# Kernel tuning notes

Measured on AMD Instinct MI355X. Metric: run time of the kernel, lower is better.

The kernel has to match this reference:

```python
import jax, jax.numpy as jnp
import numpy as np

B, DIM = 16384, 1024
H1, H2, H3 = 500, 200, 200


def setup_inputs() -> dict:
    key = jax.random.key(0)
    ks = jax.random.split(key, 16)
    s = 0.01
    return {
        "x": jax.random.normal(ks[0], (B, DIM), dtype=jnp.float32),
        "show_index": jax.random.randint(ks[1], (B,), 0, 100),
        "st": jax.random.normal(ks[2], (1000, 16), dtype=jnp.float32),
        # deep MLP params (shared across the two task heads, as in the source)
        "W1": jax.random.normal(ks[3], (DIM, H1), dtype=jnp.float32) * s,
        "b1": jnp.zeros((H1,), dtype=jnp.float32),
        "W2": jax.random.normal(ks[4], (H1, H2), dtype=jnp.float32) * s,
        "b2": jnp.zeros((H2,), dtype=jnp.float32),
        "W3": jax.random.normal(ks[5], (H2, H3), dtype=jnp.float32) * s,
        "b3": jnp.zeros((H3,), dtype=jnp.float32),
        # final sigmoid head on concat([emb(DIM), d3(H3)])
        "Wl": jax.random.normal(ks[6], (DIM + H3, 1), dtype=jnp.float32) * s,
        "bl": jnp.zeros((1,), dtype=jnp.float32),
        # per-(task, cross-layer) cross weights/biases: tf.random_normal stddev=0.01
        "cw": jax.random.normal(ks[7], (2, 3, DIM), dtype=jnp.float32) * s,
        "cb": jax.random.normal(ks[8], (2, 3, DIM), dtype=jnp.float32) * s,
    }


def reference(x, show_index, st, W1, b1, W2, b2, W3, b3, Wl, bl, cw, cb):
    # Deep part (same shared Dense layers each task -> compute once).
    d = jax.nn.relu(x @ W1 + b1)
    d = jax.nn.relu(d @ W2 + b2)
    d3 = jax.nn.relu(d @ W3 + b3)  # (B, H3)

    # cross_net: sum_i w[j] * x[b,i] * emb[b,j]  ==  x.sum(1) * emb[b,j] * w[j]
    # (collapsed form of the (B,dim,dim) outer product + axis-1 reduction)
    xsum = jnp.sum(x, axis=1, keepdims=True)  # (B, 1)
    preds = []
    for i in range(2):
        emb = x
        for j in range(3):
            emb = xsum * emb * cw[i, j] + cb[i, j] + x
        mid = jnp.concatenate([emb, d3], axis=-1)  # (B, DIM+H3)
        preds.append(jax.nn.sigmoid(mid @ Wl + bl))  # (B, 1)
    return tuple(preds)
```

## Files before the change

kernel.cpp:

```cpp
#include <hip/hip_runtime.h>
#include <hip/hip_bf16.h>
#include <math.h>

#define B_ROWS 16384
#define DIM 1024

typedef __attribute__((ext_vector_type(8))) short s16x8;
typedef __attribute__((ext_vector_type(4))) float f32x4;

static __device__ __forceinline__ unsigned short f2bf(float f) {
    union { float f; unsigned u; } v; v.f = f;
    unsigned r = v.u + 0x7FFF + ((v.u >> 16) & 1);
    return (unsigned short)(r >> 16);
}

static __device__ __forceinline__ unsigned f2fp8(float f) {
    union { float f; unsigned u; } v; v.f = f;
    const unsigned s = (v.u >> 24) & 0x80u;
    const float a = fabsf(f);
    if (a >= 448.f) return s | 0x7Eu;
    if (a < 0.015625f) {
        const int q = (int)rintf(a * 512.f);
        return s | (unsigned)q;
    }
    unsigned b = v.u & 0x7fffffffu;
    b += 0x000FFFFFu + ((b >> 20) & 1u);
    const int e = (int)(b >> 23) - 127;
    const unsigned m = (b >> 20) & 7u;
    return s | (unsigned)((e + 7) << 3) | m;
}

static __device__ __forceinline__ unsigned cvt4_fp8(float a, float b, float c, float d) {
    unsigned u;
    asm volatile("v_cvt_pk_fp8_f32 %0, %1, %2\n\t"
                 "v_cvt_pk_fp8_f32 %0, %3, %4 op_sel:[0,0,1]"
                 : "=v"(u) : "v"(a), "v"(b), "v"(c), "v"(d));
    return u;
}

static __device__ __forceinline__ void gload16(const void* g, void* l) {
    __builtin_amdgcn_global_load_lds(
        (const __attribute__((address_space(1))) unsigned int*)g,
        (__attribute__((address_space(3))) unsigned int*)l, 16, 0, 0);
}

__global__ __launch_bounds__(256, 5) void xdots_prep(
    const float* __restrict__ x,
    const float* __restrict__ W1, const float* __restrict__ W2,
    const float* __restrict__ W3,
    const float* __restrict__ cw, const float* __restrict__ cb,
    const float* __restrict__ Wl,
    unsigned char* __restrict__ W1q,
    unsigned short* __restrict__ W2b, unsigned short* __restrict__ W3b,
    float* __restrict__ czz,
    unsigned char* __restrict__ xq,
    float* __restrict__ zparts) {
    __shared__ unsigned short tile[64][72];
    __shared__ unsigned char tilec[64][72];
    __shared__ float red[4][6];
    const int tid  = threadIdx.x;
    const int lane = tid & 63;
    const int w    = tid >> 6;
    const int blk  = blockIdx.x;

    if (blk < 128) {
        const int kt = blk & 15, nt = blk >> 4;
        const int k0 = kt << 6, n0 = nt << 6;
        {
            const int r = tid >> 2, c0 = (tid & 3) << 4;
            const int kk = k0 + r;
#pragma unroll
            for (int i = 0; i < 16; ++i) {
                const int nn = n0 + c0 + i;
                const float v = (nn < 500) ? W1[(size_t)kk * 500 + nn] * 64.f : 0.f;
                tilec[r][c0 + i] = (unsigned char)f2fp8(v);
            }
        }
        __syncthreads();
        {
            const int n = tid >> 2, kc = (tid & 3) << 4;
            unsigned char* o = W1q + (size_t)(n0 + n) * 1024 + k0 + kc;
#pragma unroll
            for (int i = 0; i < 16; ++i) o[i] = tilec[kc + i][n];
        }
        return;
    } else if (blk < 176) {
        const float* src; unsigned short* dst;
        int kt, nt, Ksrc, Nsrc, ldDst;
        if (blk < 160) { kt = (blk - 128) & 7;  nt = (blk - 128) >> 3; src = W2; dst = W2b; Ksrc = 500; Nsrc = 200; ldDst = 512; }
        else           { kt = (blk - 160) & 3;  nt = (blk - 160) >> 2; src = W3; dst = W3b; Ksrc = 200; Nsrc = 200; ldDst = 256; }
        const int k0 = kt << 6, n0 = nt << 6;
        {
            const int r = tid >> 2, c0 = (tid & 3) << 4;
            const int kk = k0 + r;
#pragma unroll
            for (int i = 0; i < 16; ++i) {
                const int nn = n0 + c0 + i;
                const float v = (kk < Ksrc && nn < Nsrc) ? src[(size_t)kk * Nsrc + nn] : 0.f;
                tile[r][c0 + i] = f2bf(v);
            }
        }
        __syncthreads();
        {
            const int n = tid >> 2, kc = (tid & 3) << 4;
            unsigned short* o = dst + (size_t)(n0 + n) * ldDst + k0 + kc;
#pragma unroll
            for (int i = 0; i < 16; ++i) o[i] = tile[kc + i][n];
        }
        return;
    } else if (blk == 176) {
        float c[6] = {0.f, 0.f, 0.f, 0.f, 0.f, 0.f};
#pragma unroll
        for (int q = 0; q < 4; ++q) {
            const int k = tid * 4 + q;
            const float wl = Wl[k];
            {
                const float w2 = cw[1024 + k], w3 = cw[2048 + k];
                const float b1 = cb[k], b2 = cb[1024 + k], b3 = cb[2048 + k];
                c[0] += w2 * w3 * b1 * wl;
                c[1] += w3 * b2 * wl;
                c[2] += b3 * wl;
            }
            {
                const float w2 = cw[4096 + k], w3 = cw[5120 + k];
                const float b1 = cb[3072 + k], b2 = cb[4096 + k], b3 = cb[5120 + k];
                c[3] += w2 * w3 * b1 * wl;
                c[4] += w3 * b2 * wl;
                c[5] += b3 * wl;
            }
        }
#pragma unroll
        for (int j = 0; j < 6; ++j)
#pragma unroll
            for (int m = 1; m < 64; m <<= 1) c[j] += __shfl_xor(c[j], m, 64);
        if (lane == 0)
#pragma unroll
            for (int j = 0; j < 6; ++j) red[w][j] = c[j];
        __syncthreads();
        if (tid < 6) czz[tid] = red[0][tid] + red[1][tid] + red[2][tid] + red[3][tid];
        return;
    }

    const int row0 = (blk - 177) * 8 + (w << 1);
    float d[2][8];
#pragma unroll
    for (int r = 0; r < 2; ++r)
#pragma unroll
        for (int j = 0; j < 8; ++j) d[r][j] = 0.f;

#pragma unroll
    for (int c = 0; c < 4; ++c) {
        const int kb = c * 256 + lane * 4;
        const float4 wl4 = *(const float4*)(Wl + kb);
        const float4 c0 = *(const float4*)(cw + kb);
        const float4 c1 = *(const float4*)(cw + 1024 + kb);
        const float4 c2 = *(const float4*)(cw + 2048 + kb);
        const float4 c3 = *(const float4*)(cw + 3072 + kb);
        const float4 c4 = *(const float4*)(cw + 4096 + kb);
        const float4 c5 = *(const float4*)(cw + 5120 + kb);
        const float4 xv0 = *(const float4*)(x + (size_t)row0 * DIM + kb);
        const float4 xv1 = *(const float4*)(x + (size_t)(row0 + 1) * DIM + kb);

        const float* wlp = (const float*)&wl4;
        const float* p0 = (const float*)&c0; const float* p1 = (const float*)&c1;
        const float* p2 = (const float*)&c2; const float* p3 = (const float*)&c3;
        const float* p4 = (const float*)&c4; const float* p5 = (const float*)&c5;
        const float* xa = (const float*)&xv0; const float* xb = (const float*)&xv1;
#pragma unroll
        for (int q = 0; q < 4; ++q) {
            const float wl  = wlp[q];
            const float pa1 = p2[q] * wl;
            const float pa2 = p1[q] * pa1;
            const float pa3 = p0[q] * pa2;
            const float pb1 = p5[q] * wl;
            const float pb2 = p4[q] * pb1;
            const float pb3 = p3[q] * pb2;
            const float a = xa[q], b = xb[q];
            d[0][0] = fmaf(a, pa3, d[0][0]);
            d[0][1] = fmaf(a, pa2, d[0][1]);
            d[0][2] = fmaf(a, pa1, d[0][2]);
            d[0][3] = fmaf(a, pb3, d[0][3]);
            d[0][4] = fmaf(a, pb2, d[0][4]);
            d[0][5] = fmaf(a, pb1, d[0][5]);
            d[0][6] = fmaf(a, wl,  d[0][6]);
            d[0][7] += a;
            d[1][0] = fmaf(b, pa3, d[1][0]);
            d[1][1] = fmaf(b, pa2, d[1][1]);
            d[1][2] = fmaf(b, pa1, d[1][2]);
            d[1][3] = fmaf(b, pb3, d[1][3]);
            d[1][4] = fmaf(b, pb2, d[1][4]);
            d[1][5] = fmaf(b, pb1, d[1][5]);
            d[1][6] = fmaf(b, wl,  d[1][6]);
            d[1][7] += b;
        }
        *(unsigned*)(xq + (size_t)row0 * DIM + kb)       = cvt4_fp8(xa[0], xa[1], xa[2], xa[3]);
        *(unsigned*)(xq + (size_t)(row0 + 1) * DIM + kb) = cvt4_fp8(xb[0], xb[1], xb[2], xb[3]);
    }

#pragma unroll
    for (int r = 0; r < 2; ++r)
#pragma unroll
        for (int j = 0; j < 8; ++j)
#pragma unroll
            for (int m = 1; m < 64; m <<= 1)
                d[r][j] += __shfl_xor(d[r][j], m, 64);

    if (lane == 0) {
#pragma unroll
        for (int r = 0; r < 2; ++r) {
            float4 za = {d[r][0], d[r][1], d[r][2], d[r][3]};
            float4 zb = {d[r][4], d[r][5], d[r][6], d[r][7]};
            *(float4*)(zparts + (size_t)(row0 + r) * 8)     = za;
            *(float4*)(zparts + (size_t)(row0 + r) * 8 + 4) = zb;
        }
    }
}

static __device__ __forceinline__ void stage_fp8(
    const unsigned char* __restrict__ src, int rowBase, int kt,
    unsigned char* lds, int w, int lane) {
    const int r8   = lane >> 3;
    const int slot = lane & 7;
#pragma unroll
    for (int q = 0; q < 4; ++q) {
        const int blk   = q * 4 + w;
        const int row   = blk * 8 + r8;
        const int chunk = slot ^ (row & 7);
        gload16(src + (size_t)(rowBase + row) * 1024 + kt * 128 + chunk * 16,
                lds + blk * 1024);
    }
}

__global__ __launch_bounds__(256) void gemm_fp8(
    const unsigned char* __restrict__ A,
    const unsigned char* __restrict__ Bq,
    const float* __restrict__ bias,
    unsigned short* __restrict__ C) {
    constexpr int nK = 8;
    __shared__ unsigned char As[2][128 * 128];
    __shared__ unsigned char Bs[2][128 * 128];

    const int tid  = threadIdx.x;
    const int lane = tid & 63;
    const int wid  = tid >> 6;
    const int wm   = wid >> 1;
    const int wn   = wid & 1;
    const int g    = lane >> 4;
    const int r16  = lane & 15;

    const int cpx = gridDim.x >> 3;
    const int swz = (blockIdx.x & 7) * cpx + (blockIdx.x >> 3);
    const int rowBase = (swz >> 2) << 7;
    const int colBase = (swz & 3) << 7;

    f32x4 acc[4][4];
#pragma unroll
    for (int m = 0; m < 4; ++m)
#pragma unroll
        for (int n = 0; n < 4; ++n)
            acc[m][n] = (f32x4){0.f, 0.f, 0.f, 0.f};

    stage_fp8(A, rowBase, 0, As[0], wid, lane);
    stage_fp8(Bq, colBase, 0, Bs[0], wid, lane);
    asm volatile("s_waitcnt vmcnt(0)" ::: "memory");
    __builtin_amdgcn_s_barrier();
    asm volatile("" ::: "memory");

    for (int kt = 0; kt < nK; ++kt) {
        const int buf = kt & 1;
        if (kt + 1 < nK) {
            stage_fp8(A, rowBase, kt + 1, As[buf ^ 1], wid, lane);
            stage_fp8(Bq, colBase, kt + 1, Bs[buf ^ 1], wid, lane);
        }
        asm volatile("" ::: "memory");

        const unsigned char* Ab = As[buf];
        const unsigned char* Bb = Bs[buf];
#pragma unroll
        for (int ks = 0; ks < 4; ++ks) {
            long af[4], bf[4];
#pragma unroll
            for (int m = 0; m < 4; ++m) {
                const int row = wm * 64 + m * 16 + r16;
                const int byte = row * 128 +
                    ((((ks << 1) | (g >> 1)) ^ (row & 7)) << 4) + ((g & 1) << 3);
                af[m] = *(const long*)(Ab + byte);
            }
#pragma unroll
            for (int n = 0; n < 4; ++n) {
                const int row = wn * 64 + n * 16 + r16;
                const int byte = row * 128 +
                    ((((ks << 1) | (g >> 1)) ^ (row & 7)) << 4) + ((g & 1) << 3);
                bf[n] = *(const long*)(Bb + byte);
            }
#pragma unroll
            for (int m = 0; m < 4; ++m)
#pragma unroll
                for (int n = 0; n < 4; ++n)
                    acc[m][n] = __builtin_amdgcn_mfma_f32_16x16x32_fp8_fp8(
                        af[m], bf[n], acc[m][n], 0, 0, 0);
        }

        asm volatile("s_waitcnt vmcnt(0)" ::: "memory");
        __builtin_amdgcn_s_barrier();
        asm volatile("" ::: "memory");
    }

    unsigned short* Cb = (unsigned short*)As[0];
#pragma unroll
    for (int n = 0; n < 4; ++n) {
        const int lcol = wn * 64 + n * 16 + r16;
        const int col = colBase + lcol;
        const float bv = (col < 500) ? bias[col] : 0.f;
#pragma unroll
        for (int m = 0; m < 4; ++m) {
            const int lrow = wm * 64 + m * 16 + g * 4;
#pragma unroll
            for (int r = 0; r < 4; ++r) {
                float v = acc[m][n][r] * 0.015625f + bv;
                v = v > 0.f ? v : 0.f;
                Cb[(lrow + r) * 128 + lcol] = f2bf(v);
            }
        }
    }
    __syncthreads();

    {
        const int row  = tid >> 1;
        const int half = tid & 1;
        const uint4* s = (const uint4*)(Cb + row * 128 + half * 64);
        uint4* dd = (uint4*)(C + (size_t)(rowBase + row) * 512 + colBase + half * 64);
        dd[0] = s[0]; dd[1] = s[1]; dd[2] = s[2]; dd[3] = s[3];
    }
}

template <int ROWS>
static __device__ __forceinline__ void stage8(
    const unsigned short* __restrict__ src, int K, int rowBase, int kt,
    unsigned short* lds, int w, int lane) {
    const int r8   = lane >> 3;
    const int slot = lane & 7;
#pragma unroll
    for (int q = 0; q < ROWS / 64; ++q) {
        const int blk   = q * 8 + w;
        const int row   = blk * 8 + r8;
        const int chunk = slot ^ (row & 7);
        gload16(src + (size_t)(rowBase + row) * K + kt * 64 + chunk * 8,
                lds + blk * 512);
    }
}

__global__ __launch_bounds__(512) void tail_fused(
    const unsigned short* __restrict__ d1,
    const unsigned short* __restrict__ W2b, const float* __restrict__ b2,
    const unsigned short* __restrict__ W3b, const float* __restrict__ b3,
    const float* __restrict__ Wl, const float* __restrict__ bl,
    const float* __restrict__ zparts, const float* __restrict__ czz,
    float* __restrict__ out) {
    __shared__ unsigned short As[2][64 * 64];
    __shared__ unsigned short Bs[2][256 * 64];
    __shared__ unsigned short P[64 * 256];
    __shared__ float part[8][64];

    const int tid  = threadIdx.x;
    const int lane = tid & 63;
    const int wid  = tid >> 6;
    const int wm   = wid >> 2;
    const int wn   = wid & 3;
    const int g    = lane >> 4;
    const int r16  = lane & 15;
    const int rowBase = blockIdx.x << 6;

    f32x4 acc[2][4];
#pragma unroll
    for (int m = 0; m < 2; ++m)
#pragma unroll
        for (int n = 0; n < 4; ++n)
            acc[m][n] = (f32x4){0.f, 0.f, 0.f, 0.f};

    stage8<64>(d1, 512, rowBase, 0, As[0], wid, lane);
    stage8<256>(W2b, 512, 0, 0, Bs[0], wid, lane);

    for (int kt = 0; kt < 8; ++kt) {
        const int buf = kt & 1;
        if (kt + 1 < 8) {
            stage8<64>(d1, 512, rowBase, kt + 1, As[buf ^ 1], wid, lane);
            stage8<256>(W2b, 512, 0, kt + 1, Bs[buf ^ 1], wid, lane);
            asm volatile("s_waitcnt vmcnt(5)" ::: "memory");
        } else {
            asm volatile("s_waitcnt vmcnt(0)" ::: "memory");
        }
        __builtin_amdgcn_s_barrier();
        asm volatile("" ::: "memory");

        const unsigned short* Ab = As[buf];
        const unsigned short* Bb = Bs[buf];
#pragma unroll
        for (int ks = 0; ks < 2; ++ks) {
            s16x8 af[2], bfr[4];
#pragma unroll
            for (int m = 0; m < 2; ++m) {
                const int row = wm * 32 + m * 16 + r16;
                const int off = ((ks * 4 + g) * 16) ^ ((row & 7) << 4);
                af[m] = *(const s16x8*)((const char*)Ab + row * 128 + off);
            }
#pragma unroll
            for (int n = 0; n < 4; ++n) {
                const int row = wn * 64 + n * 16 + r16;
                const int off = ((ks * 4 + g) * 16) ^ ((row & 7) << 4);
                bfr[n] = *(const s16x8*)((const char*)Bb + row * 128 + off);
            }
#pragma unroll
            for (int m = 0; m < 2; ++m)
#pragma unroll
                for (int n = 0; n < 4; ++n)
                    acc[m][n] = __builtin_amdgcn_mfma_f32_16x16x32_bf16(af[m], bfr[n], acc[m][n], 0, 0, 0);
        }
        asm volatile("s_waitcnt lgkmcnt(0)" ::: "memory");
        __builtin_amdgcn_s_barrier();
        asm volatile("" ::: "memory");
    }

#pragma unroll
    for (int n = 0; n < 4; ++n) {
        const int col = wn * 64 + n * 16 + r16;
        const float bv = (col < 200) ? b2[col] : 0.f;
#pragma unroll
        for (int m = 0; m < 2; ++m) {
#pragma unroll
            for (int r = 0; r < 4; ++r) {
                const int row = wm * 32 + m * 16 + g * 4 + r;
                float v = acc[m][n][r] + bv;
                v = v > 0.f ? v : 0.f;
                const int byte = row * 512 + ((col * 2) ^ ((row & 7) << 4));
                *(unsigned short*)((char*)P + byte) = f2bf(v);
            }
        }
    }

    stage8<256>(W3b, 256, 0, 0, Bs[0], wid, lane);
    asm volatile("s_waitcnt lgkmcnt(0)" ::: "memory");
    __builtin_amdgcn_s_barrier();
    asm volatile("" ::: "memory");

    f32x4 acc2[2][4];
#pragma unroll
    for (int m = 0; m < 2; ++m)
#pragma unroll
        for (int n = 0; n < 4; ++n)
            acc2[m][n] = (f32x4){0.f, 0.f, 0.f, 0.f};

    for (int kt = 0; kt < 4; ++kt) {
        const int buf = kt & 1;
        if (kt + 1 < 4) {
            stage8<256>(W3b, 256, 0, kt + 1, Bs[buf ^ 1], wid, lane);
            asm volatile("s_waitcnt vmcnt(4)" ::: "memory");
        } else {
            asm volatile("s_waitcnt vmcnt(0)" ::: "memory");
        }
        __builtin_amdgcn_s_barrier();
        asm volatile("" ::: "memory");

        const unsigned short* Bb = Bs[buf];
#pragma unroll
        for (int ks = 0; ks < 2; ++ks) {
            s16x8 af[2], bfr[4];
#pragma unroll
            for (int m = 0; m < 2; ++m) {
                const int row = wm * 32 + m * 16 + r16;
                const int byte = row * 512 + ((kt * 128 + (ks * 4 + g) * 16) ^ ((row & 7) << 4));
                af[m] = *(const s16x8*)((const char*)P + byte);
            }
#pragma unroll
            for (int n = 0; n < 4; ++n) {
                const int row = wn * 64 + n * 16 + r16;
                const int off = ((ks * 4 + g) * 16) ^ ((row & 7) << 4);
                bfr[n] = *(const s16x8*)((const char*)Bb + row * 128 + off);
            }
#pragma unroll
            for (int m = 0; m < 2; ++m)
#pragma unroll
                for (int n = 0; n < 4; ++n)
                    acc2[m][n] = __builtin_amdgcn_mfma_f32_16x16x32_bf16(af[m], bfr[n], acc2[m][n], 0, 0, 0);
        }
        asm volatile("s_waitcnt lgkmcnt(0)" ::: "memory");
        __builtin_amdgcn_s_barrier();
        asm volatile("" ::: "memory");
    }

    float wlv[4], b3v[4];
#pragma unroll
    for (int n = 0; n < 4; ++n) {
        const int col = wn * 64 + n * 16 + r16;
        wlv[n] = (col < 200) ? Wl[1024 + col] : 0.f;
        b3v[n] = (col < 200) ? b3[col] : 0.f;
    }
#pragma unroll
    for (int m = 0; m < 2; ++m) {
#pragma unroll
        for (int r = 0; r < 4; ++r) {
            float s = 0.f;
#pragma unroll
            for (int n = 0; n < 4; ++n) {
                float v = acc2[m][n][r] + b3v[n];
                v = v > 0.f ? v : 0.f;
                s += v * wlv[n];
            }
            s += __shfl_xor(s, 1, 64);
            s += __shfl_xor(s, 2, 64);
            s += __shfl_xor(s, 4, 64);
            s += __shfl_xor(s, 8, 64);
            if (r16 == 0) part[wid][wm * 32 + m * 16 + g * 4 + r] = s;
        }
    }
    __syncthreads();

    if (tid < 64) {
        const int row = rowBase + tid;
        const int wmr = (tid >> 5) << 2;
        const float t = part[wmr][tid] + part[wmr + 1][tid] +
                        part[wmr + 2][tid] + part[wmr + 3][tid];
        const float blv = bl[0];
        const float* zp = zparts + (size_t)row * 8;
        float4 zpa = *(const float4*)(zp);
        float4 zpb = *(const float4*)(zp + 4);
        const float s = zpb.w;
        const float z0 = ((zpa.x * s + zpa.y + czz[0]) * s + zpa.z + czz[1]) * s
                         + zpb.z + czz[2] + t + blv;
        const float z1 = ((zpa.w * s + zpb.x + czz[3]) * s + zpb.y + czz[4]) * s
                         + zpb.z + czz[5] + t + blv;
        out[row]          = 1.f / (1.f + expf(-z0));
        out[B_ROWS + row] = 1.f / (1.f + expf(-z1));
    }
}

extern "C" void kernel_launch(void* const* d_in, const int* in_sizes, int n_in,
                              void* d_out, int out_size, void* d_ws, size_t ws_size,
                              hipStream_t stream) {
    const float* x  = (const float*)d_in[0];
    const float* W1 = (const float*)d_in[3];
    const float* b1 = (const float*)d_in[4];
    const float* W2 = (const float*)d_in[5];
    const float* b2 = (const float*)d_in[6];
    const float* W3 = (const float*)d_in[7];
    const float* b3 = (const float*)d_in[8];
    const float* Wl = (const float*)d_in[9];
    const float* bl = (const float*)d_in[10];
    const float* cw = (const float*)d_in[11];
    const float* cb = (const float*)d_in[12];
    float* out = (float*)d_out;

    unsigned short* d1  = (unsigned short*)d_ws;
    unsigned char*  xq  = (unsigned char*)(d1 + (size_t)16384 * 512);
    unsigned char*  W1q = xq + (size_t)16384 * 1024;
    unsigned short* W2b = (unsigned short*)(W1q + (size_t)512 * 1024);
    unsigned short* W3b = W2b + (size_t)256 * 512;
    float* zparts = (float*)(W3b + (size_t)256 * 256);
    float* czz = zparts + (size_t)16384 * 8;

    xdots_prep<<<177 + 2048, 256, 0, stream>>>(
        x, W1, W2, W3, cw, cb, Wl, W1q, W2b, W3b, czz, xq, zparts);

    gemm_fp8<<<512, 256, 0, stream>>>(xq, W1q, b1, d1);

    tail_fused<<<256, 512, 0, stream>>>(d1, W2b, b2, W3b, b3, Wl, bl,
                                        zparts, czz, out);
}
```

Before: 54.44 us.

## Quantize layers two and three to fp8 and precompute cross-weight products in LDS

Layer-2 and layer-3 weights are now stored as scaled fp8 instead of bf16. The layer-1 output is written as fp8, and the tail kernel uses fp8 MFMA with half as many K iterations and half the staging traffic. The x-dot prep blocks now build the per-column cross-weight product table once in shared memory rather than recomputing it from global loads every chunk. This cuts memory traffic for the d1 intermediate and the weights, at the cost of more quantization error in the hidden activations.

```diff
diff --git a/kernel.cpp b/kernel.cpp
--- a/kernel.cpp
+++ b/kernel.cpp
@@ -5,7 +5,6 @@
 #define B_ROWS 16384
 #define DIM 1024
 
-typedef __attribute__((ext_vector_type(8))) short s16x8;
 typedef __attribute__((ext_vector_type(4))) float f32x4;
 
 static __device__ __forceinline__ unsigned short f2bf(float f) {
@@ -37,6 +36,11 @@
                  : "=v"(u) : "v"(a), "v"(b), "v"(c), "v"(d));
     return u;
 }
+static __device__ __forceinline__ unsigned cvt2_fp8(float a, float b) {
+    unsigned u = 0;
+    asm volatile("v_cvt_pk_fp8_f32 %0, %1, %2" : "+v"(u) : "v"(a), "v"(b));
+    return u;
+}
 
 static __device__ __forceinline__ void gload16(const void* g, void* l) {
     __builtin_amdgcn_global_load_lds(
@@ -51,20 +55,23 @@
     const float* __restrict__ cw, const float* __restrict__ cb,
     const float* __restrict__ Wl,
     unsigned char* __restrict__ W1q,
-    unsigned short* __restrict__ W2b, unsigned short* __restrict__ W3b,
+    unsigned char* __restrict__ W2q, unsigned char* __restrict__ W3q,
     float* __restrict__ czz,
     unsigned char* __restrict__ xq,
     float* __restrict__ zparts) {
-    __shared__ unsigned short tile[64][72];
-    __shared__ unsigned char tilec[64][72];
-    __shared__ float red[4][6];
+    __shared__ __align__(16) char smem[7 * 4096];
     const int tid  = threadIdx.x;
     const int lane = tid & 63;
     const int w    = tid >> 6;
     const int blk  = blockIdx.x;
 
-    if (blk < 128) {
-        const int kt = blk & 15, nt = blk >> 4;
+    if (blk < 176) {
+        unsigned char* tilec = (unsigned char*)smem;
+        const float* src; unsigned char* dst;
+        int kt, nt, Ksrc, Nsrc, ldDst;
+        if (blk < 128)      { kt = blk & 15;         nt = blk >> 4;         src = W1; dst = W1q; Ksrc = 1024; Nsrc = 500; ldDst = 1024; }
+        else if (blk < 160) { kt = (blk - 128) & 7;  nt = (blk - 128) >> 3; src = W2; dst = W2q; Ksrc = 500;  Nsrc = 200; ldDst = 512;  }
+        else                { kt = (blk - 160) & 3;  nt = (blk - 160) >> 2; src = W3; dst = W3q; Ksrc = 200;  Nsrc = 200; ldDst = 256;  }
         const int k0 = kt << 6, n0 = nt << 6;
         {
             const int r = tid >> 2, c0 = (tid & 3) << 4;
@@ -72,43 +79,20 @@
 #pragma unroll
             for (int i = 0; i < 16; ++i) {
                 const int nn = n0 + c0 + i;
-                const float v = (nn < 500) ? W1[(size_t)kk * 500 + nn] * 64.f : 0.f;
-                tilec[r][c0 + i] = (unsigned char)f2fp8(v);
+                const float v = (kk < Ksrc && nn < Nsrc) ? src[(size_t)kk * Nsrc + nn] * 64.f : 0.f;
+                tilec[r * 72 + c0 + i] = (unsigned char)f2fp8(v);
             }
         }
         __syncthreads();
         {
             const int n = tid >> 2, kc = (tid & 3) << 4;
-            unsigned char* o = W1q + (size_t)(n0 + n) * 1024 + k0 + kc;
-#pragma unroll
-            for (int i = 0; i < 16; ++i) o[i] = tilec[kc + i][n];
-        }
-        return;
-    } else if (blk < 176) {
-        const float* src; unsigned short* dst;
-        int kt, nt, Ksrc, Nsrc, ldDst;
-        if (blk < 160) { kt = (blk - 128) & 7;  nt = (blk - 128) >> 3; src = W2; dst = W2b; Ksrc = 500; Nsrc = 200; ldDst = 512; }
-        else           { kt = (blk - 160) & 3;  nt = (blk - 160) >> 2; src = W3; dst = W3b; Ksrc = 200; Nsrc = 200; ldDst = 256; }
-        const int k0 = kt << 6, n0 = nt << 6;
-        {
-            const int r = tid >> 2, c0 = (tid & 3) << 4;
-            const int kk = k0 + r;
-#pragma unroll
-            for (int i = 0; i < 16; ++i) {
-                const int nn = n0 + c0 + i;
-                const float v = (kk < Ksrc && nn < Nsrc) ? src[(size_t)kk * Nsrc + nn] : 0.f;
-                tile[r][c0 + i] = f2bf(v);
-            }
-        }
-        __syncthreads();
-        {
-            const int n = tid >> 2, kc = (tid & 3) << 4;
-            unsigned short* o = dst + (size_t)(n0 + n) * ldDst + k0 + kc;
-#pragma unroll
-            for (int i = 0; i < 16; ++i) o[i] = tile[kc + i][n];
+            unsigned char* o = dst + (size_t)(n0 + n) * ldDst + k0 + kc;
+#pragma unroll
+            for (int i = 0; i < 16; ++i) o[i] = tilec[(kc + i) * 72 + n];
         }
         return;
     } else if (blk == 176) {
+        float* red = (float*)(smem + 20480);
         float c[6] = {0.f, 0.f, 0.f, 0.f, 0.f, 0.f};
 #pragma unroll
         for (int q = 0; q < 4; ++q) {
@@ -135,11 +119,38 @@
             for (int m = 1; m < 64; m <<= 1) c[j] += __shfl_xor(c[j], m, 64);
         if (lane == 0)
 #pragma unroll
-            for (int j = 0; j < 6; ++j) red[w][j] = c[j];
+            for (int j = 0; j < 6; ++j) red[w * 6 + j] = c[j];
         __syncthreads();
-        if (tid < 6) czz[tid] = red[0][tid] + red[1][tid] + red[2][tid] + red[3][tid];
+        if (tid < 6) czz[tid] = red[tid] + red[6 + tid] + red[12 + tid] + red[18 + tid];
         return;
     }
+
+    float* tbl = (float*)smem;
+    {
+        const int k = tid * 4;
+        const float4 wl4 = *(const float4*)(Wl + k);
+        const float4 c0 = *(const float4*)(cw + k);
+        const float4 c1 = *(const float4*)(cw + 1024 + k);
+        const float4 c2 = *(const float4*)(cw + 2048 + k);
+        const float4 c3 = *(const float4*)(cw + 3072 + k);
+        const float4 c4 = *(const float4*)(cw + 4096 + k);
+        const float4 c5 = *(const float4*)(cw + 5120 + k);
+        float4 pa1, pa2, pa3, pb1, pb2, pb3;
+        pa1.x = c2.x * wl4.x; pa1.y = c2.y * wl4.y; pa1.z = c2.z * wl4.z; pa1.w = c2.w * wl4.w;
+        pa2.x = c1.x * pa1.x; pa2.y = c1.y * pa1.y; pa2.z = c1.z * pa1.z; pa2.w = c1.w * pa1.w;
+        pa3.x = c0.x * pa2.x; pa3.y = c0.y * pa2.y; pa3.z = c0.z * pa2.z; pa3.w = c0.w * pa2.w;
+        pb1.x = c5.x * wl4.x; pb1.y = c5.y * wl4.y; pb1.z = c5.z * wl4.z; pb1.w = c5.w * wl4.w;
+        pb2.x = c4.x * pb1.x; pb2.y = c4.y * pb1.y; pb2.z = c4.z * pb1.z; pb2.w = c4.w * pb1.w;
+        pb3.x = c3.x * pb2.x; pb3.y = c3.y * pb2.y; pb3.z = c3.z * pb2.z; pb3.w = c3.w * pb2.w;
+        *(float4*)(tbl + k)        = pa3;
+        *(float4*)(tbl + 1024 + k) = pa2;
+        *(float4*)(tbl + 2048 + k) = pa1;
+        *(float4*)(tbl + 3072 + k) = pb3;
+        *(float4*)(tbl + 4096 + k) = pb2;
+        *(float4*)(tbl + 5120 + k) = pb1;
+        *(float4*)(tbl + 6144 + k) = wl4;
+    }
+    __syncthreads();
 
     const int row0 = (blk - 177) * 8 + (w << 1);
     float d[2][8];
@@ -151,50 +162,28 @@
 #pragma unroll
     for (int c = 0; c < 4; ++c) {
         const int kb = c * 256 + lane * 4;
-        const float4 wl4 = *(const float4*)(Wl + kb);
-        const float4 c0 = *(const float4*)(cw + kb);
-        const float4 c1 = *(const float4*)(cw + 1024 + kb);
-        const float4 c2 = *(const float4*)(cw + 2048 + kb);
-        const float4 c3 = *(const float4*)(cw + 3072 + kb);
-        const float4 c4 = *(const float4*)(cw + 4096 + kb);
-        const float4 c5 = *(const float4*)(cw + 5120 + kb);
         const float4 xv0 = *(const float4*)(x + (size_t)row0 * DIM + kb);
         const float4 xv1 = *(const float4*)(x + (size_t)(row0 + 1) * DIM + kb);
-
-        const float* wlp = (const float*)&wl4;
-        const float* p0 = (const float*)&c0; const float* p1 = (const float*)&c1;
-        const float* p2 = (const float*)&c2; const float* p3 = (const float*)&c3;
-        const float* p4 = (const float*)&c4; const float* p5 = (const float*)&c5;
-        const float* xa = (const float*)&xv0; const float* xb = (const float*)&xv1;
-#pragma unroll
-        for (int q = 0; q < 4; ++q) {
-            const float wl  = wlp[q];
-            const float pa1 = p2[q] * wl;
-            const float pa2 = p1[q] * pa1;
-            const float pa3 = p0[q] * pa2;
-            const float pb1 = p5[q] * wl;
-            const float pb2 = p4[q] * pb1;
-            const float pb3 = p3[q] * pb2;
-            const float a = xa[q], b = xb[q];
-            d[0][0] = fmaf(a, pa3, d[0][0]);
-            d[0][1] = fmaf(a, pa2, d[0][1]);
-            d[0][2] = fmaf(a, pa1, d[0][2]);
-            d[0][3] = fmaf(a, pb3, d[0][3]);
-            d[0][4] = fmaf(a, pb2, d[0][4]);
-            d[0][5] = fmaf(a, pb1, d[0][5]);
-            d[0][6] = fmaf(a, wl,  d[0][6]);
-            d[0][7] += a;
-            d[1][0] = fmaf(b, pa3, d[1][0]);
-            d[1][1] = fmaf(b, pa2, d[1][1]);
-            d[1][2] = fmaf(b, pa1, d[1][2]);
-            d[1][3] = fmaf(b, pb3, d[1][3]);
-            d[1][4] = fmaf(b, pb2, d[1][4]);
-            d[1][5] = fmaf(b, pb1, d[1][5]);
-            d[1][6] = fmaf(b, wl,  d[1][6]);
-            d[1][7] += b;
-        }
-        *(unsigned*)(xq + (size_t)row0 * DIM + kb)       = cvt4_fp8(xa[0], xa[1], xa[2], xa[3]);
-        *(unsigned*)(xq + (size_t)(row0 + 1) * DIM + kb) = cvt4_fp8(xb[0], xb[1], xb[2], xb[3]);
+        float4 t[7];
+#pragma unroll
+        for (int j = 0; j < 7; ++j) t[j] = *(const float4*)(tbl + j * 1024 + kb);
+
+#pragma unroll
+        for (int j = 0; j < 7; ++j) {
+            d[0][j] = fmaf(xv0.x, t[j].x, d[0][j]);
+            d[0][j] = fmaf(xv0.y, t[j].y, d[0][j]);
+            d[0][j] = fmaf(xv0.z, t[j].z, d[0][j]);
+            d[0][j] = fmaf(xv0.w, t[j].w, d[0][j]);
+            d[1][j] = fmaf(xv1.x, t[j].x, d[1][j]);
+            d[1][j] = fmaf(xv1.y, t[j].y, d[1][j]);
+            d[1][j] = fmaf(xv1.z, t[j].z, d[1][j]);
+            d[1][j] = fmaf(xv1.w, t[j].w, d[1][j]);
+        }
+        d[0][7] += xv0.x + xv0.y + xv0.z + xv0.w;
+        d[1][7] += xv1.x + xv1.y + xv1.z + xv1.w;
+
+        *(unsigned*)(xq + (size_t)row0 * DIM + kb)       = cvt4_fp8(xv0.x, xv0.y, xv0.z, xv0.w);
+        *(unsigned*)(xq + (size_t)(row0 + 1) * DIM + kb) = cvt4_fp8(xv1.x, xv1.y, xv1.z, xv1.w);
     }
 
 #pragma unroll
@@ -231,11 +220,27 @@
     }
 }
 
+template <int ROWS>
+static __device__ __forceinline__ void stage_fp8w8(
+    const unsigned char* __restrict__ src, int K, int rowBase, int kt,
+    unsigned char* lds, int w, int lane) {
+    const int r8   = lane >> 3;
+    const int slot = lane & 7;
+#pragma unroll
+    for (int q = 0; q < ROWS / 64; ++q) {
+        const int blk   = q * 8 + w;
+        const int row   = blk * 8 + r8;
+        const int chunk = slot ^ (row & 7);
+        gload16(src + (size_t)(rowBase + row) * K + kt * 128 + chunk * 16,
+                lds + blk * 1024);
+    }
+}
+
 __global__ __launch_bounds__(256) void gemm_fp8(
     const unsigned char* __restrict__ A,
     const unsigned char* __restrict__ Bq,
     const float* __restrict__ bias,
-    unsigned short* __restrict__ C) {
+    unsigned char* __restrict__ C) {
     constexpr int nK = 8;
     __shared__ unsigned char As[2][128 * 128];
     __shared__ unsigned char Bs[2][128 * 128];
@@ -306,7 +311,7 @@
         asm volatile("" ::: "memory");
     }
 
-    unsigned short* Cb = (unsigned short*)As[0];
+    unsigned char* Cb = As[0];
 #pragma unroll
     for (int n = 0; n < 4; ++n) {
         const int lcol = wn * 64 + n * 16 + r16;
@@ -315,12 +320,16 @@
 #pragma unroll
         for (int m = 0; m < 4; ++m) {
             const int lrow = wm * 64 + m * 16 + g * 4;
-#pragma unroll
-            for (int r = 0; r < 4; ++r) {
-                float v = acc[m][n][r] * 0.015625f + bv;
-                v = v > 0.f ? v : 0.f;
-                Cb[(lrow + r) * 128 + lcol] = f2bf(v);
-            }
+            float v0 = acc[m][n][0] * 0.015625f + bv; v0 = v0 > 0.f ? v0 : 0.f;
+            float v1 = acc[m][n][1] * 0.015625f + bv; v1 = v1 > 0.f ? v1 : 0.f;
+            float v2 = acc[m][n][2] * 0.015625f + bv; v2 = v2 > 0.f ? v2 : 0.f;
+            float v3 = acc[m][n][3] * 0.015625f + bv; v3 = v3 > 0.f ? v3 : 0.f;
+            const unsigned u01 = cvt2_fp8(v0, v1);
+            const unsigned u23 = cvt2_fp8(v2, v3);
+            Cb[(lrow + 0) * 128 + lcol] = (unsigned char)(u01 & 0xff);
+            Cb[(lrow + 1) * 128 + lcol] = (unsigned char)((u01 >> 8) & 0xff);
+            Cb[(lrow + 2) * 128 + lcol] = (unsigned char)(u23 & 0xff);
+            Cb[(lrow + 3) * 128 + lcol] = (unsigned char)((u23 >> 8) & 0xff);
         }
     }
     __syncthreads();
@@ -334,32 +343,18 @@
     }
 }
 
-template <int ROWS>
-static __device__ __forceinline__ void stage8(
-    const unsigned short* __restrict__ src, int K, int rowBase, int kt,
-    unsigned short* lds, int w, int lane) {
-    const int r8   = lane >> 3;
-    const int slot = lane & 7;
-#pragma unroll
-    for (int q = 0; q < ROWS / 64; ++q) {
-        const int blk   = q * 8 + w;
-        const int row   = blk * 8 + r8;
-        const int chunk = slot ^ (row & 7);
-        gload16(src + (size_t)(rowBase + row) * K + kt * 64 + chunk * 8,
-                lds + blk * 512);
-    }
-}
-
-__global__ __launch_bounds__(512) void tail_fused(
-    const unsigned short* __restrict__ d1,
-    const unsigned short* __restrict__ W2b, const float* __restrict__ b2,
-    const unsigned short* __restrict__ W3b, const float* __restrict__ b3,
+__global__ __launch_bounds__(512) void tail_fp8(
+    const unsigned char* __restrict__ d1q,
+    const unsigned char* __restrict__ W2q,
+    const float* __restrict__ b2,
+    const unsigned char* __restrict__ W3q,
+    const float* __restrict__ b3,
     const float* __restrict__ Wl, const float* __restrict__ bl,
     const float* __restrict__ zparts, const float* __restrict__ czz,
     float* __restrict__ out) {
-    __shared__ unsigned short As[2][64 * 64];
-    __shared__ unsigned short Bs[2][256 * 64];
-    __shared__ unsigned short P[64 * 256];
+    __shared__ unsigned char As[2][64 * 128];
+    __shared__ unsigned char Bs[2][256 * 128];
+    __shared__ unsigned char P[64 * 256];
     __shared__ float part[8][64];
 
     const int tid  = threadIdx.x;
@@ -378,14 +373,14 @@
         for (int n = 0; n < 4; ++n)
             acc[m][n] = (f32x4){0.f, 0.f, 0.f, 0.f};
 
-    stage8<64>(d1, 512, rowBase, 0, As[0], wid, lane);
-    stage8<256>(W2b, 512, 0, 0, Bs[0], wid, lane);
-
-    for (int kt = 0; kt < 8; ++kt) {
+    stage_fp8w8<64>(d1q, 512, rowBase, 0, As[0], wid, lane);
+    stage_fp8w8<256>(W2q, 512, 0, 0, Bs[0], wid, lane);
+
+    for (int kt = 0; kt < 4; ++kt) {
         const int buf = kt & 1;
-        if (kt + 1 < 8) {
-            stage8<64>(d1, 512, rowBase, kt + 1, As[buf ^ 1], wid, lane);
-            stage8<256>(W2b, 512, 0, kt + 1, Bs[buf ^ 1], wid, lane);
+        if (kt + 1 < 4) {
+            stage_fp8w8<64>(d1q, 512, rowBase, kt + 1, As[buf ^ 1], wid, lane);
+            stage_fp8w8<256>(W2q, 512, 0, kt + 1, Bs[buf ^ 1], wid, lane);
             asm volatile("s_waitcnt vmcnt(5)" ::: "memory");
         } else {
             asm volatile("s_waitcnt vmcnt(0)" ::: "memory");
@@ -393,28 +388,31 @@
         __builtin_amdgcn_s_barrier();
         asm volatile("" ::: "memory");
 
-        const unsigned short* Ab = As[buf];
-        const unsigned short* Bb = Bs[buf];
-#pragma unroll
-        for (int ks = 0; ks < 2; ++ks) {
-            s16x8 af[2], bfr[4];
+        const unsigned char* Ab = As[buf];
+        const unsigned char* Bb = Bs[buf];
+#pragma unroll
+        for (int ks = 0; ks < 4; ++ks) {
+            long af[2], bf[4];
 #pragma unroll
             for (int m = 0; m < 2; ++m) {
                 const int row = wm * 32 + m * 16 + r16;
-                const int off = ((ks * 4 + g) * 16) ^ ((row & 7) << 4);
-                af[m] = *(const s16x8*)((const char*)Ab + row * 128 + off);
+                const int byte = row * 128 +
+                    ((((ks << 1) | (g >> 1)) ^ (row & 7)) << 4) + ((g & 1) << 3);
+                af[m] = *(const long*)(Ab + byte);
             }
 #pragma unroll
             for (int n = 0; n < 4; ++n) {
                 const int row = wn * 64 + n * 16 + r16;
-                const int off = ((ks * 4 + g) * 16) ^ ((row & 7) << 4);
-                bfr[n] = *(const s16x8*)((const char*)Bb + row * 128 + off);
+                const int byte = row * 128 +
+                    ((((ks << 1) | (g >> 1)) ^ (row & 7)) << 4) + ((g & 1) << 3);
+                bf[n] = *(const long*)(Bb + byte);
             }
 #pragma unroll
             for (int m = 0; m < 2; ++m)
 #pragma unroll
                 for (int n = 0; n < 4; ++n)
-                    acc[m][n] = __builtin_amdgcn_mfma_f32_16x16x32_bf16(af[m], bfr[n], acc[m][n], 0, 0, 0);
+                    acc[m][n] = __builtin_amdgcn_mfma_f32_16x16x32_fp8_fp8(
+                        af[m], bf[n], acc[m][n], 0, 0, 0);
         }
         asm volatile("s_waitcnt lgkmcnt(0)" ::: "memory");
         __builtin_amdgcn_s_barrier();
@@ -427,21 +425,26 @@
         const float bv = (col < 200) ? b2[col] : 0.f;
 #pragma unroll
         for (int m = 0; m < 2; ++m) {
+            const int lrow = wm * 32 + m * 16 + g * 4;
+            float v0 = acc[m][n][0] * 0.015625f + bv; v0 = v0 > 0.f ? v0 : 0.f;
+            float v1 = acc[m][n][1] * 0.015625f + bv; v1 = v1 > 0.f ? v1 : 0.f;
+            float v2 = acc[m][n][2] * 0.015625f + bv; v2 = v2 > 0.f ? v2 : 0.f;
+            float v3 = acc[m][n][3] * 0.015625f + bv; v3 = v3 > 0.f ? v3 : 0.f;
+            const unsigned u01 = cvt2_fp8(v0, v1);
+            const unsigned u23 = cvt2_fp8(v2, v3);
+            const int cpos = col >> 4, clo = col & 15;
 #pragma unroll
             for (int r = 0; r < 4; ++r) {
-                const int row = wm * 32 + m * 16 + g * 4 + r;
-                float v = acc[m][n][r] + bv;
-                v = v > 0.f ? v : 0.f;
-                const int byte = row * 512 + ((col * 2) ^ ((row & 7) << 4));
-                *(unsigned short*)((char*)P + byte) = f2bf(v);
-            }
-        }
-    }
-
-    stage8<256>(W3b, 256, 0, 0, Bs[0], wid, lane);
+                const int row = lrow + r;
+                const unsigned byteV = (r < 2) ? ((r == 0) ? u01 : (u01 >> 8))
+                                               : ((r == 2) ? u23 : (u23 >> 8));
+                P[row * 256 + ((cpos ^ (row & 7)) << 4) + clo] = (unsigned char)(byteV & 0xff);
+            }
+        }
+    }
     asm volatile("s_waitcnt lgkmcnt(0)" ::: "memory");
-    __builtin_amdgcn_s_barrier();
-    asm volatile("" ::: "memory");
+
+    stage_fp8w8<256>(W3q, 256, 0, 0, Bs[0], wid, lane);
 
     f32x4 acc2[2][4];
 #pragma unroll
@@ -450,10 +453,10 @@
         for (int n = 0; n < 4; ++n)
             acc2[m][n] = (f32x4){0.f, 0.f, 0.f, 0.f};
 
-    for (int kt = 0; kt < 4; ++kt) {
+    for (int kt = 0; kt < 2; ++kt) {
         const int buf = kt & 1;
-        if (kt + 1 < 4) {
-            stage8<256>(W3b, 256, 0, kt + 1, Bs[buf ^ 1], wid, lane);
+        if (kt + 1 < 2) {
+            stage_fp8w8<256>(W3q, 256, 0, kt + 1, Bs[buf ^ 1], wid, lane);
             asm volatile("s_waitcnt vmcnt(4)" ::: "memory");
         } else {
             asm volatile("s_waitcnt vmcnt(0)" ::: "memory");
@@ -461,27 +464,30 @@
         __builtin_amdgcn_s_barrier();
         asm volatile("" ::: "memory");
 
-        const unsigned short* Bb = Bs[buf];
-#pragma unroll
-        for (int ks = 0; ks < 2; ++ks) {
-            s16x8 af[2], bfr[4];
+        const unsigned char* Bb = Bs[buf];
+#pragma unroll
+        for (int ks = 0; ks < 4; ++ks) {
+            long af[2], bf[4];
 #pragma unroll
             for (int m = 0; m < 2; ++m) {
                 const int row = wm * 32 + m * 16 + r16;
-                const int byte = row * 512 + ((kt * 128 + (ks * 4 + g) * 16) ^ ((row & 7) << 4));
-                af[m] = *(const s16x8*)((const char*)P + byte);
+                const int byte = row * 256 +
+                    (((kt * 8 + ((ks << 1) | (g >> 1))) ^ (row & 7)) << 4) + ((g & 1) << 3);
+                af[m] = *(const long*)(P + byte);
             }
 #pragma unroll
             for (int n = 0; n < 4; ++n) {
                 const int row = wn * 64 + n * 16 + r16;
-                const int off = ((ks * 4 + g) * 16) ^ ((row & 7) << 4);
-                bfr[n] = *(const s16x8*)((const char*)Bb + row * 128 + off);
+                const int byte = row * 128 +
+                    ((((ks << 1) | (g >> 1)) ^ (row & 7)) << 4) + ((g & 1) << 3);
+                bf[n] = *(const long*)(Bb + byte);
             }
 #pragma unroll
             for (int m = 0; m < 2; ++m)
 #pragma unroll
                 for (int n = 0; n < 4; ++n)
-                    acc2[m][n] = __builtin_amdgcn_mfma_f32_16x16x32_bf16(af[m], bfr[n], acc2[m][n], 0, 0, 0);
+                    acc2[m][n] = __builtin_amdgcn_mfma_f32_16x16x32_fp8_fp8(
+                        af[m], bf[n], acc2[m][n], 0, 0, 0);
         }
         asm volatile("s_waitcnt lgkmcnt(0)" ::: "memory");
         __builtin_amdgcn_s_barrier();
@@ -502,7 +508,7 @@
             float s = 0.f;
 #pragma unroll
             for (int n = 0; n < 4; ++n) {
-                float v = acc2[m][n][r] + b3v[n];
+                float v = acc2[m][n][r] * 0.015625f + b3v[n];
                 v = v > 0.f ? v : 0.f;
                 s += v * wlv[n];
             }
@@ -550,19 +556,19 @@
     const float* cb = (const float*)d_in[12];
     float* out = (float*)d_out;
 
-    unsigned short* d1  = (unsigned short*)d_ws;
-    unsigned char*  xq  = (unsigned char*)(d1 + (size_t)16384 * 512);
-    unsigned char*  W1q = xq + (size_t)16384 * 1024;
-    unsigned short* W2b = (unsigned short*)(W1q + (size_t)512 * 1024);
-    unsigned short* W3b = W2b + (size_t)256 * 512;
-    float* zparts = (float*)(W3b + (size_t)256 * 256);
+    unsigned char* d1q = (unsigned char*)d_ws;
+    unsigned char* xq  = d1q + (size_t)16384 * 512;
+    unsigned char* W1q = xq + (size_t)16384 * 1024;
+    unsigned char* W2q = W1q + (size_t)512 * 1024;
+    unsigned char* W3q = W2q + (size_t)256 * 512;
+    float* zparts = (float*)(W3q + (size_t)256 * 256);
     float* czz = zparts + (size_t)16384 * 8;
 
     xdots_prep<<<177 + 2048, 256, 0, stream>>>(
-        x, W1, W2, W3, cw, cb, Wl, W1q, W2b, W3b, czz, xq, zparts);
-
-    gemm_fp8<<<512, 256, 0, stream>>>(xq, W1q, b1, d1);
-
-    tail_fused<<<256, 512, 0, stream>>>(d1, W2b, b2, W3b, b3, Wl, bl,
-                                        zparts, czz, out);
-}
+        x, W1, W2, W3, cw, cb, Wl, W1q, W2q, W3q, czz, xq, zparts);
+
+    gemm_fp8<<<512, 256, 0, stream>>>(xq, W1q, b1, d1q);
+
+    tail_fp8<<<256, 512, 0, stream>>>(d1q, W2q, b2, W3q, b3, Wl, bl,
+                                      zparts, czz, out);
+}
```

Measured after the change: 64.60 us. +18.6%, slower.
